# Optimization experiments

Hardware: AMD Instinct MI355X
Metric: run time of the kernel (lower is better)

The kernel has to match this reference:

```python
import jax, jax.numpy as jnp
import numpy as np

MAXDISP = 48  # module stores maxdisp + 1 = 49 disparity planes


def setup_inputs() -> dict:
    key = jax.random.key(0)
    k1, k2 = jax.random.split(key)
    B, C, H, W = 4, 320, 128, 240
    x = jax.random.normal(k1, (B, C, H, W), dtype=jnp.float32)
    y = jax.random.normal(k2, (B, C, H, W), dtype=jnp.float32)
    return {"x": x, "y": y}


def _cost_volume(x, y, maxdisp):
    # x, y: [B, C, H, W]. For each disparity i: channel-sum correlation of
    # x shifted right against y, left-padded with zeros to width W.
    b, c, h, w = x.shape
    D = maxdisp + 1
    costs = [(x * y).sum(axis=1)]  # [B, H, W], disparity 0
    for i in range(1, D):
        corr = (x[:, :, :, i:] * y[:, :, :, : w - i]).sum(axis=1)  # [B, H, W-i]
        costs.append(jnp.pad(corr, ((0, 0), (0, 0), (i, 0))))
    # torch cats [1,B,H,W] slices along dim 1 (disp-major) then unsqueeze(0)
    cost = jnp.stack(costs, axis=0)            # [D, B, H, W]
    return cost.reshape(1, 1, D * b, h, w)     # [1, 1, D*B, H, W]


def reference(x, y):
    return _cost_volume(x, y, MAXDISP)
```

## Files before the change

### kernel.cpp

```cpp
#include <hip/hip_runtime.h>
#include <stdint.h>
#include <stddef.h>

#define NB 4
#define NC 320
#define NH 128
#define NW 240
#define ND 49
#define HW (NH * NW)
#define CC 32
#define NCHUNK (NC / CC)

typedef float f32x4 __attribute__((ext_vector_type(4)));
typedef short s16x8 __attribute__((ext_vector_type(8)));

__device__ __forceinline__ uint32_t bf16r(float f) {
  uint32_t u = __builtin_bit_cast(uint32_t, f);
  return (u + 0x7FFFu + ((u >> 16) & 1u)) >> 16;
}

__device__ __forceinline__ int swz(int w) { return (w ^ (w >> 2)) & 3; }

__global__ __launch_bounds__(256, 2) void cv_kernel(const float* __restrict__ X,
                                                    const float* __restrict__ Y,
                                                    float* __restrict__ O) {
  __shared__ short lds[2 * 2 * NW * CC];

  const int tid = threadIdx.x;
  const int row = blockIdx.x;
  const int b = row >> 7, h = row & 127;
  const float* xrow = X + (size_t)b * NC * HW + (size_t)h * NW;
  const float* yrow = Y + (size_t)b * NC * HW + (size_t)h * NW;

  const int wave = tid >> 6;
  const int l = tid & 63;
  const int m = l & 15;
  const int q = l >> 4;

  f32x4 acc[4][4] = {};
  float sv[2][4][8];

  auto stage_load = [&](int chunk) {
    if (tid < NW) {
#pragma unroll
      for (int arr = 0; arr < 2; ++arr) {
        const float* src = arr ? yrow : xrow;
#pragma unroll
        for (int c8 = 0; c8 < 4; ++c8) {
          const float* p = src + (size_t)(chunk * CC + c8 * 8) * HW + tid;
#pragma unroll
          for (int j = 0; j < 8; ++j) sv[arr][c8][j] = p[(size_t)j * HW];
        }
      }
    }
  };

  auto stage_write = [&](int buf) {
    if (tid < NW) {
      const int w = tid, sw = swz(w);
#pragma unroll
      for (int arr = 0; arr < 2; ++arr) {
#pragma unroll
        for (int c8 = 0; c8 < 4; ++c8) {
          s16x8 s;
#pragma unroll
          for (int j = 0; j < 8; ++j) s[j] = (short)bf16r(sv[arr][c8][j]);
          *(s16x8*)&lds[((buf * 2 + arr) * NW + w) * CC + ((c8 ^ sw) * 8)] = s;
        }
      }
    }
  };

  auto compute = [&](int buf) {
#pragma unroll
    for (int i = 0; i < 4; ++i) {
      const int wt = wave + 4 * i;
      if (wt <= 14) {
        const int wa = wt * 16 + m;
        const s16x8 a =
            *(const s16x8*)&lds[((buf * 2 + 0) * NW + wa) * CC + ((q ^ swz(wa)) * 8)];
#pragma unroll
        for (int ss = 0; ss < 4; ++ss) {
          const int st = wt - 3 + ss;
          if (st >= 0) {
            const int wb = st * 16 + m;
            const s16x8 bb =
                *(const s16x8*)&lds[((buf * 2 + 1) * NW + wb) * CC + ((q ^ swz(wb)) * 8)];
            acc[i][ss] = __builtin_amdgcn_mfma_f32_16x16x32_bf16(a, bb, acc[i][ss], 0, 0, 0);
          }
        }
      }
    }
  };

  stage_load(0);
  stage_write(0);
  __syncthreads();

  for (int k = 0; k < NCHUNK; ++k) {
    if (k + 1 < NCHUNK) stage_load(k + 1);
    compute(k & 1);
    if (k + 1 < NCHUNK) stage_write((k + 1) & 1);
    __syncthreads();
  }

  float* orow = O + ((size_t)b * NH + h) * NW;
#pragma unroll
  for (int i = 0; i < 4; ++i) {
    const int wt = wave + 4 * i;
    if (wt > 14) continue;
#pragma unroll
    for (int ss = 0; ss < 4; ++ss) {
      const int st = wt - 3 + ss;
      const int wj = st * 16 + m;
#pragma unroll
      for (int r = 0; r < 4; ++r) {
        const int wi = wt * 16 + q * 4 + r;
        const int d = wi - wj;
        if (d >= 0 && d < ND) {
          const float v = (st >= 0) ? acc[i][ss][r] : 0.0f;
          orow[(size_t)d * (NB * HW) + wi] = v;
        }
      }
    }
  }
}

extern "C" void kernel_launch(void* const* d_in, const int* in_sizes, int n_in,
                              void* d_out, int out_size, void* d_ws, size_t ws_size,
                              hipStream_t stream) {
  const float* x = (const float*)d_in[0];
  const float* y = (const float*)d_in[1];
  float* out = (float*)d_out;
  cv_kernel<<<dim3(512), dim3(256), 0, stream>>>(x, y, out);
}
```

Baseline: 73.12 us.

## Stage fp32 rows via async global_load_lds and convert to bf16 at MFMA time

Replaces the register-staged load, bf16 convert and LDS write with direct global-to-LDS 16-byte async loads of fp32 channel rows, double-buffered with vmcnt waits and raw barriers. Conversion to bf16 moves into the compute loop using v_cvt_pk_bf16_f32 on scalar LDS reads, with a rotated per-channel layout to spread bank accesses. It also remaps block IDs to interleave rows across the grid and drops the 2-blocks-per-CU launch bound. The cost is twice the LDS footprint (fp32), more LDS reads per MFMA operand, and possible loss of occupancy.

New measurement: 82.41 us. 1.13x slower.

```diff
diff --git a/kernel.cpp b/kernel.cpp
--- a/kernel.cpp
+++ b/kernel.cpp
@@ -10,104 +10,120 @@
 #define HW (NH * NW)
 #define CC 32
 #define NCHUNK (NC / CC)
+#define ROWF 240
+#define ROWS 64
+#define BUFWORDS (ROWS * ROWF)
+#define CBYTES ((size_t)CC * HW * 4)
 
 typedef float f32x4 __attribute__((ext_vector_type(4)));
 typedef short s16x8 __attribute__((ext_vector_type(8)));
 
-__device__ __forceinline__ uint32_t bf16r(float f) {
-  uint32_t u = __builtin_bit_cast(uint32_t, f);
-  return (u + 0x7FFFu + ((u >> 16) & 1u)) >> 16;
+__device__ __forceinline__ void gload_lds16(const void* g, void* l) {
+  __builtin_amdgcn_global_load_lds(
+      (const __attribute__((address_space(1))) void*)g,
+      (__attribute__((address_space(3))) void*)l, 16, 0, 0);
 }
 
-__device__ __forceinline__ int swz(int w) { return (w ^ (w >> 2)) & 3; }
+template <int N> __device__ __forceinline__ void waitcnt_vm() {
+  asm volatile("s_waitcnt vmcnt(%0)" ::"i"(N) : "memory");
+  __builtin_amdgcn_sched_barrier(0);
+}
 
-__global__ __launch_bounds__(256, 2) void cv_kernel(const float* __restrict__ X,
-                                                    const float* __restrict__ Y,
-                                                    float* __restrict__ O) {
-  __shared__ short lds[2 * 2 * NW * CC];
+__device__ __forceinline__ s16x8 pack8(const float* f) {
+  union { uint32_t u[4]; s16x8 v; } r;
+#pragma unroll
+  for (int t = 0; t < 4; ++t)
+    asm("v_cvt_pk_bf16_f32 %0, %1, %2"
+        : "=v"(r.u[t]) : "v"(f[2 * t]), "v"(f[2 * t + 1]));
+  return r.v;
+}
 
+__global__ __launch_bounds__(256) void cv_kernel(const float* __restrict__ X,
+                                                 const float* __restrict__ Y,
+                                                 float* __restrict__ O) {
+  __shared__ float lds[2 * BUFWORDS];
   const int tid = threadIdx.x;
-  const int row = blockIdx.x;
-  const int b = row >> 7, h = row & 127;
-  const float* xrow = X + (size_t)b * NC * HW + (size_t)h * NW;
-  const float* yrow = Y + (size_t)b * NC * HW + (size_t)h * NW;
-
   const int wave = tid >> 6;
   const int l = tid & 63;
   const int m = l & 15;
   const int q = l >> 4;
 
+  const int bid = blockIdx.x;
+  const int logical = (bid & 7) * 64 + (bid >> 3);
+  const int b = logical >> 7, h = logical & 127;
+  const float* xrow = X + (size_t)b * NC * HW + (size_t)h * NW;
+  const float* yrow = Y + (size_t)b * NC * HW + (size_t)h * NW;
+  float* orow = O + ((size_t)b * NH + h) * NW;
+
+  const char* pv[16];
+  int loff[16];
+#pragma unroll
+  for (int ii = 0; ii < 16; ++ii) {
+    const int r = wave * 16 + ii;
+    const int cl = r & 31;
+    int lu = l + 2 * (cl >> 3);
+    if (lu >= 60) lu -= 60;
+    pv[ii] = (const char*)((r < 32 ? xrow : yrow) + (size_t)cl * HW + lu * 4);
+    loff[ii] = r * ROWF;
+  }
+
+  auto issue = [&](int buf) {
+    if (l < 60) {
+#pragma unroll
+      for (int ii = 0; ii < 16; ++ii) {
+        gload_lds16(pv[ii], lds + buf * BUFWORDS + loff[ii]);
+        pv[ii] += CBYTES;
+      }
+    }
+  };
+
   f32x4 acc[4][4] = {};
-  float sv[2][4][8];
 
-  auto stage_load = [&](int chunk) {
-    if (tid < NW) {
+  auto compute = [&](int buf) {
+    const float* BX = lds + buf * BUFWORDS;
+    const float* BY = BX + 32 * ROWF;
 #pragma unroll
-      for (int arr = 0; arr < 2; ++arr) {
-        const float* src = arr ? yrow : xrow;
+    for (int it = 0; it < 4; ++it) {
+      const int wt = wave + it * 4;
+      if (wt > 14) continue;
+      float fa[8];
+      int o4a = 4 * wt + (m >> 2) - 2 * q; if (o4a < 0) o4a += 60;
+      const int oa = o4a * 4 + (m & 3);
 #pragma unroll
-        for (int c8 = 0; c8 < 4; ++c8) {
-          const float* p = src + (size_t)(chunk * CC + c8 * 8) * HW + tid;
+      for (int t = 0; t < 8; ++t) fa[t] = BX[(8 * q + t) * ROWF + oa];
+      const s16x8 a = pack8(fa);
 #pragma unroll
-          for (int j = 0; j < 8; ++j) sv[arr][c8][j] = p[(size_t)j * HW];
+      for (int ss = 0; ss < 4; ++ss) {
+        const int st = wt - 3 + ss;
+        if (st >= 0) {
+          float fb[8];
+          int o4b = 4 * st + (m >> 2) - 2 * q; if (o4b < 0) o4b += 60;
+          const int ob = o4b * 4 + (m & 3);
+#pragma unroll
+          for (int t = 0; t < 8; ++t) fb[t] = BY[(8 * q + t) * ROWF + ob];
+          const s16x8 bb = pack8(fb);
+          acc[it][ss] = __builtin_amdgcn_mfma_f32_16x16x32_bf16(a, bb, acc[it][ss], 0, 0, 0);
         }
       }
     }
   };
 
-  auto stage_write = [&](int buf) {
-    if (tid < NW) {
-      const int w = tid, sw = swz(w);
-#pragma unroll
-      for (int arr = 0; arr < 2; ++arr) {
-#pragma unroll
-        for (int c8 = 0; c8 < 4; ++c8) {
-          s16x8 s;
-#pragma unroll
-          for (int j = 0; j < 8; ++j) s[j] = (short)bf16r(sv[arr][c8][j]);
-          *(s16x8*)&lds[((buf * 2 + arr) * NW + w) * CC + ((c8 ^ sw) * 8)] = s;
-        }
-      }
+  issue(0);
+  for (int k = 0; k < NCHUNK; ++k) {
+    __builtin_amdgcn_s_barrier();
+    if (k + 1 < NCHUNK) {
+      issue((k + 1) & 1);
+      waitcnt_vm<16>();
+    } else {
+      waitcnt_vm<0>();
     }
-  };
-
-  auto compute = [&](int buf) {
-#pragma unroll
-    for (int i = 0; i < 4; ++i) {
-      const int wt = wave + 4 * i;
-      if (wt <= 14) {
-        const int wa = wt * 16 + m;
-        const s16x8 a =
-            *(const s16x8*)&lds[((buf * 2 + 0) * NW + wa) * CC + ((q ^ swz(wa)) * 8)];
-#pragma unroll
-        for (int ss = 0; ss < 4; ++ss) {
-          const int st = wt - 3 + ss;
-          if (st >= 0) {
-            const int wb = st * 16 + m;
-            const s16x8 bb =
-                *(const s16x8*)&lds[((buf * 2 + 1) * NW + wb) * CC + ((q ^ swz(wb)) * 8)];
-            acc[i][ss] = __builtin_amdgcn_mfma_f32_16x16x32_bf16(a, bb, acc[i][ss], 0, 0, 0);
-          }
-        }
-      }
-    }
-  };
-
-  stage_load(0);
-  stage_write(0);
-  __syncthreads();
-
-  for (int k = 0; k < NCHUNK; ++k) {
-    if (k + 1 < NCHUNK) stage_load(k + 1);
+    __builtin_amdgcn_s_barrier();
     compute(k & 1);
-    if (k + 1 < NCHUNK) stage_write((k + 1) & 1);
-    __syncthreads();
   }
 
-  float* orow = O + ((size_t)b * NH + h) * NW;
 #pragma unroll
-  for (int i = 0; i < 4; ++i) {
-    const int wt = wave + 4 * i;
+  for (int it = 0; it < 4; ++it) {
+    const int wt = wave + it * 4;
     if (wt > 14) continue;
 #pragma unroll
     for (int ss = 0; ss < 4; ++ss) {
@@ -118,7 +134,7 @@
         const int wi = wt * 16 + q * 4 + r;
         const int d = wi - wj;
         if (d >= 0 && d < ND) {
-          const float v = (st >= 0) ? acc[i][ss][r] : 0.0f;
+          const float v = (st >= 0) ? acc[it][ss][r] : 0.0f;
           orow[(size_t)d * (NB * HW) + wi] = v;
         }
       }
```
